# Kernel tuning notes

Hardware: AMD Instinct MI355X
Metric: run time of the kernel (lower is better)

Reference implementation:

```python
import jax, jax.numpy as jnp
import numpy as np

B, L, D = 4, 4096, 128
BLOCK, SPARSITY = 64, 0.9
NEG = -1e9


def _make_block_mask(key):
    nb = L // BLOCK
    bm = jax.random.uniform(key, (nb, nb)) > SPARSITY
    bm = bm | jnp.eye(nb, dtype=bool)  # keep diagonal blocks so no row is fully masked
    bm = jnp.tril(bm)
    return jnp.repeat(jnp.repeat(bm, BLOCK, axis=0), BLOCK, axis=1)  # [L, L]


def _xavier(key, shape):
    limit = float(np.sqrt(6.0 / (shape[0] + shape[1])))
    return jax.random.uniform(key, shape, jnp.float32, -limit, limit)


def setup_inputs() -> dict:
    key = jax.random.key(0)
    ks = jax.random.split(key, 10)
    t = lambda k: jax.random.normal(k, (B, L, D), jnp.float32)
    return {
        'q_real': t(ks[0]), 'q_imag': t(ks[1]),
        'k_real': t(ks[2]), 'k_imag': t(ks[3]),
        'v_real': t(ks[4]), 'v_imag': t(ks[5]),
        'W_qkv': _xavier(ks[6], (6 * D, 6 * D)),
        'b_qkv': jnp.zeros((6 * D,), jnp.float32),
        'W_out': _xavier(ks[7], (2 * D, 2 * D)),
        'b_out': jnp.zeros((2 * D,), jnp.float32),
        'block_mask': _make_block_mask(ks[8]),
    }


def reference(q_real, q_imag, k_real, k_imag, v_real, v_imag,
              W_qkv, b_qkv, W_out, b_out, block_mask):
    d = q_real.shape[-1]
    scale = d ** -0.5
    # fused qkv projection over the 6 concatenated channels
    x = jnp.concatenate([q_real, q_imag, k_real, k_imag, v_real, v_imag], axis=-1)  # [B,L,6D]
    qkv = (x @ W_qkv.T + b_qkv).reshape(x.shape[0], x.shape[1], 6, d)
    q_r, q_i, k_r, k_i, v_r, v_i = (qkv[:, :, j] for j in range(6))

    def attn(q, k, v):
        s = jnp.einsum('bqd,bkd->bqk', q, k) * scale          # [B,L,L]
        s = jnp.where(block_mask[None], s, NEG)               # block-sparse mask
        a = jax.nn.softmax(s, axis=-1)                        # dropout = identity (eval)
        return jnp.einsum('bqk,bkd->bqd', a, v)

    out = jnp.concatenate([attn(q_r, k_r, v_r), attn(q_i, k_i, v_i)], axis=-1)  # [B,L,2D]
    out = out @ W_out.T + b_out
    return out[..., :d], out[..., d:]
```

## Files before the change

### kernel.cpp

```cpp
#include <hip/hip_runtime.h>
#include <hip/hip_bf16.h>

typedef unsigned short u16;
typedef __attribute__((ext_vector_type(8))) short bf16x8;
typedef __attribute__((ext_vector_type(4))) float f32x4;

#define SEQ_L 4096
#define M_TOT 16384

__device__ __forceinline__ float bf2f(u16 x) {
    unsigned u = ((unsigned)x) << 16;
    return __builtin_bit_cast(float, u);
}
__device__ __forceinline__ u16 f2bf(float f) {
    unsigned u = __builtin_bit_cast(unsigned, f);
    u += 0x7FFFu + ((u >> 16) & 1u);
    return (u16)(u >> 16);
}
__device__ __forceinline__ void gload16(const u16* g, u16* l) {
    __builtin_amdgcn_global_load_lds(
        (const __attribute__((address_space(1))) unsigned int*)g,
        (__attribute__((address_space(3))) unsigned int*)l, 16, 0, 0);
}

__global__ __launch_bounds__(256) void prep_all(
    const float* __restrict__ in0, const float* __restrict__ in1, const float* __restrict__ in2,
    const float* __restrict__ in3, const float* __restrict__ in4, const float* __restrict__ in5,
    const float* __restrict__ Wqkv, const float* __restrict__ Wout, const void* __restrict__ mask,
    u16* __restrict__ x, u16* __restrict__ Wqkv_bf, u16* __restrict__ Wout_bf,
    unsigned long long* __restrict__ bmap) {
    int id = blockIdx.x * 256 + threadIdx.x;
    if (id < 1572864) {
        const float* ins[6] = {in0, in1, in2, in3, in4, in5};
        int which = id >> 18, j = id & 262143;
        int m = j >> 4, c8 = j & 15;
        const float* sp = ins[which] + (size_t)m * 128 + c8 * 8;
        float4 a = *(const float4*)sp;
        float4 b = *(const float4*)(sp + 4);
        u16 t[8] = {f2bf(a.x), f2bf(a.y), f2bf(a.z), f2bf(a.w),
                    f2bf(b.x), f2bf(b.y), f2bf(b.z), f2bf(b.w)};
        *(uint4*)(x + (size_t)m * 768 + which * 128 + c8 * 8) = *(uint4*)t;
    } else if (id < 1572864 + 73728 + 8192) {
        int i = id - 1572864;
        const float* src = (i < 73728) ? Wqkv : Wout;
        u16* dst = (i < 73728) ? Wqkv_bf : Wout_bf;
        if (i >= 73728) i -= 73728;
        const float* sp = src + (size_t)i * 8;
        float4 a = *(const float4*)sp;
        float4 b = *(const float4*)(sp + 4);
        u16 t[8] = {f2bf(a.x), f2bf(a.y), f2bf(a.z), f2bf(a.w),
                    f2bf(b.x), f2bf(b.y), f2bf(b.z), f2bf(b.w)};
        *(uint4*)(dst + (size_t)i * 8) = *(uint4*)t;
    } else if (id < 1572864 + 73728 + 8192 + 4096) {
        int i = id - 1572864 - 73728 - 8192;
        int bi = i >> 6, bj = i & 63;
        size_t e = (size_t)(bi * 64) * SEQ_L + (size_t)bj * 64;
        const unsigned char* p8 = (const unsigned char*)mask;
        unsigned w0 = *(const unsigned*)mask;
        bool v;
        if (w0 == 0x01010101u || w0 == 0xFFFFFFFFu)      v = p8[e] != 0;
        else if (w0 == 0x3F803F80u || w0 == 0x3C003C00u) v = ((const u16*)mask)[e] != 0;
        else                                             v = ((const unsigned*)mask)[e] != 0;
        unsigned long long bits = __ballot(v);
        if ((i & 63) == 0) bmap[bi] = bits;
    }
}

__global__ __launch_bounds__(256, 3) void qkv_gemm(
    const u16* __restrict__ X, const u16* __restrict__ W, const float* __restrict__ bias,
    u16* __restrict__ qk, u16* __restrict__ vt) {
    __shared__ __align__(16) u16 As[128 * 64];
    __shared__ __align__(16) u16 Bs[128 * 64];
    int m0 = blockIdx.x * 128, n0 = blockIdx.y * 128;
    int tid = threadIdx.x, lane = tid & 63, w = tid >> 6;
    int ln = lane & 15, quad = lane >> 4;
    int rw = (w >> 1) * 64, cw = (w & 1) * 64;
    int lr8 = lane >> 3, lc = lane & 7;
    f32x4 acc[4][4] = {};
    for (int kk = 0; kk < 768; kk += 64) {
        __syncthreads();
        #pragma unroll
        for (int j = 0; j < 4; j++) {
            int r0 = w * 32 + j * 8, r = r0 + lr8;
            gload16(X + (size_t)(m0 + r) * 768 + kk + ((lc ^ (r & 7)) * 8), As + r0 * 64 + lane * 8);
            gload16(W + (size_t)(n0 + r) * 768 + kk + ((lc ^ (r & 7)) * 8), Bs + r0 * 64 + lane * 8);
        }
        __syncthreads();
        #pragma unroll
        for (int s = 0; s < 2; s++) {
            bf16x8 af[4], bfr[4];
            #pragma unroll
            for (int i = 0; i < 4; i++) {
                int R = rw + i * 16 + ln;
                af[i] = *(const bf16x8*)(As + R * 64 + ((4 * s + quad) ^ (ln & 7)) * 8);
            }
            #pragma unroll
            for (int t = 0; t < 4; t++) {
                int R = cw + t * 16 + ln;
                bfr[t] = *(const bf16x8*)(Bs + R * 64 + ((4 * s + quad) ^ (ln & 7)) * 8);
            }
            #pragma unroll
            for (int i = 0; i < 4; i++)
                #pragma unroll
                for (int t = 0; t < 4; t++)
                    acc[i][t] = __builtin_amdgcn_mfma_f32_16x16x32_bf16(af[i], bfr[t], acc[i][t], 0, 0, 0);
        }
    }
    if (n0 < 512) {
        #pragma unroll
        for (int i = 0; i < 4; i++) {
            int row0 = m0 + rw + i * 16 + 4 * quad;
            #pragma unroll
            for (int t = 0; t < 4; t++) {
                int col = n0 + cw + t * 16 + ln;
                float bv = bias[col];
                #pragma unroll
                for (int r = 0; r < 4; r++)
                    qk[(size_t)(row0 + r) * 512 + col] = f2bf(acc[i][t][r] + bv);
            }
        }
    } else {
        #pragma unroll
        for (int i = 0; i < 4; i++) {
            int row0 = m0 + rw + i * 16 + 4 * quad;
            int b = row0 >> 12, seq = row0 & 4095;
            #pragma unroll
            for (int t = 0; t < 4; t++) {
                int col = n0 + cw + t * 16 + ln;
                float bv = bias[col];
                int d = col - 512;
                u16 pk[4] = {f2bf(acc[i][t][0] + bv), f2bf(acc[i][t][1] + bv),
                             f2bf(acc[i][t][2] + bv), f2bf(acc[i][t][3] + bv)};
                *(ushort4*)(vt + ((size_t)(b * 2 + (d >> 7)) * 128 + (d & 127)) * SEQ_L + seq)
                    = *(ushort4*)pk;
            }
        }
    }
}

__global__ __launch_bounds__(256, 2) void attn_sparse(
    const u16* __restrict__ qk, const u16* __restrict__ vt,
    const unsigned long long* __restrict__ bmap, u16* __restrict__ attn_bf) {
    __shared__ __align__(16) u16 Ks[2][64 * 128];
    __shared__ __align__(16) u16 Vs[2][128 * 64];

    int lane = threadIdx.x & 63, w = threadIdx.x >> 6;
    int ln = lane & 15, quad = lane >> 4;
    int u = blockIdx.x >> 3, v = blockIdx.x & 7;
    int qi = (u < 32) ? (63 - u) : (u - 32);
    int b = v >> 1, ch = v & 1;
    int rowbase = b * SEQ_L + qi * 64 + w * 16;
    const float scale = 0.08838834764831845f;

    bf16x8 qf[4];
    {
        const u16* qp = qk + (size_t)(rowbase + ln) * 512 + ch * 128;
        #pragma unroll
        for (int s = 0; s < 4; s++) qf[s] = *(const bf16x8*)(qp + 32 * s + 8 * quad);
    }

    float m_st = -1e30f, l_st = 0.f;
    f32x4 accO[8] = {};

    const u16* kbase0 = qk + (size_t)b * SEQ_L * 512 + 256 + ch * 128;
    const u16* vbase0 = vt + (size_t)(b * 2 + ch) * 128 * SEQ_L;
    unsigned long long bm = bmap[qi];

    int kb = __ffsll(bm) - 1; bm &= bm - 1;
    {
        const u16* kp = kbase0 + (size_t)(kb * 64) * 512;
        const u16* vp = vbase0 + kb * 64;
        #pragma unroll
        for (int j = 0; j < 4; j++) {
            int kr = w * 16 + j * 4 + (lane >> 4);
            gload16(kp + (size_t)kr * 512 + (((lane & 15) ^ (kr & 7)) * 8),
                    Ks[0] + (w * 16 + j * 4) * 128 + lane * 8);
        }
        #pragma unroll
        for (int j = 0; j < 4; j++) {
            int d = w * 32 + j * 8 + (lane >> 3);
            gload16(vp + (size_t)d * SEQ_L + (((lane & 7) ^ (d & 7)) * 8),
                    Vs[0] + (w * 32 + j * 8) * 64 + lane * 8);
        }
    }

    int srcA = ln + ((quad & 1) << 5);
    int srcB = srcA + 16;
    bool hi = (quad & 2) != 0;

    int bufc = 0;
    while (true) {
        int nkb = -1;
        if (bm) {
            nkb = __ffsll(bm) - 1; bm &= bm - 1;
            const u16* kp = kbase0 + (size_t)(nkb * 64) * 512;
            const u16* vp = vbase0 + nkb * 64;
            u16* Kd = Ks[bufc ^ 1];
            u16* Vd = Vs[bufc ^ 1];
            #pragma unroll
            for (int j = 0; j < 4; j++) {
                int kr = w * 16 + j * 4 + (lane >> 4);
                gload16(kp + (size_t)kr * 512 + (((lane & 15) ^ (kr & 7)) * 8),
                        Kd + (w * 16 + j * 4) * 128 + lane * 8);
            }
            #pragma unroll
            for (int j = 0; j < 4; j++) {
                int d = w * 32 + j * 8 + (lane >> 3);
                gload16(vp + (size_t)d * SEQ_L + (((lane & 7) ^ (d & 7)) * 8),
                        Vd + (w * 32 + j * 8) * 64 + lane * 8);
            }
        }
        if (nkb >= 0) __builtin_amdgcn_s_waitcnt(0x0F78);
        else          __builtin_amdgcn_s_waitcnt(0x0F70);
        __builtin_amdgcn_s_barrier();

        const u16* K = Ks[bufc];
        const u16* V = Vs[bufc];

        f32x4 accS[4] = {};
        #pragma unroll
        for (int s = 0; s < 4; s++)
            #pragma unroll
            for (int t = 0; t < 4; t++) {
                bf16x8 kf = *(const bf16x8*)(K + (t * 16 + ln) * 128 +
                                             (((4 * s + quad) ^ (ln & 7)) * 8));
                accS[t] = __builtin_amdgcn_mfma_f32_16x16x32_bf16(kf, qf[s], accS[t], 0, 0, 0);
            }

        float mx = fmaxf(fmaxf(fmaxf(accS[0][0], accS[0][1]), fmaxf(accS[0][2], accS[0][3])),
                         fmaxf(fmaxf(fmaxf(accS[1][0], accS[1][1]), fmaxf(accS[1][2], accS[1][3])),
                               fmaxf(fmaxf(fmaxf(accS[2][0], accS[2][1]), fmaxf(accS[2][2], accS[2][3])),
                                     fmaxf(fmaxf(accS[3][0], accS[3][1]), fmaxf(accS[3][2], accS[3][3])))));
        mx = fmaxf(mx, __shfl_xor(mx, 16, 64));
        mx = fmaxf(mx, __shfl_xor(mx, 32, 64));
        float nm = fmaxf(m_st, mx * scale);
        float alpha = __expf(m_st - nm);
        m_st = nm;

        float p[4][4];
        float rs = 0.f;
        #pragma unroll
        for (int t = 0; t < 4; t++)
            #pragma unroll
            for (int r = 0; r < 4; r++) {
                p[t][r] = __expf(accS[t][r] * scale - nm);
                rs += p[t][r];
            }
        rs += __shfl_xor(rs, 16, 64);
        rs += __shfl_xor(rs, 32, 64);
        l_st = l_st * alpha + rs;

        unsigned uA[4], uB[4];
        #pragma unroll
        for (int t = 0; t < 4; t++) {
            uA[t] = (unsigned)f2bf(p[t][0]) | ((unsigned)f2bf(p[t][1]) << 16);
            uB[t] = (unsigned)f2bf(p[t][2]) | ((unsigned)f2bf(p[t][3]) << 16);
        }

        float al[4];
        #pragma unroll
        for (int r = 0; r < 4; r++) al[r] = __shfl(alpha, 4 * quad + r, 64);
        #pragma unroll
        for (int nt = 0; nt < 8; nt++)
            #pragma unroll
            for (int r = 0; r < 4; r++) accO[nt][r] *= al[r];

        #pragma unroll
        for (int h = 0; h < 2; h++) {
            unsigned a0 = (unsigned)__shfl((int)uA[2 * h], srcA, 64);
            unsigned a1 = (unsigned)__shfl((int)uA[2 * h + 1], srcA, 64);
            unsigned b0 = (unsigned)__shfl((int)uB[2 * h], srcA, 64);
            unsigned b1 = (unsigned)__shfl((int)uB[2 * h + 1], srcA, 64);
            unsigned c0 = (unsigned)__shfl((int)uA[2 * h], srcB, 64);
            unsigned c1 = (unsigned)__shfl((int)uA[2 * h + 1], srcB, 64);
            unsigned d0 = (unsigned)__shfl((int)uB[2 * h], srcB, 64);
            unsigned d1 = (unsigned)__shfl((int)uB[2 * h + 1], srcB, 64);
            union { unsigned w4[4]; bf16x8 v; } pu;
            pu.w4[0] = hi ? a1 : a0;
            pu.w4[1] = hi ? b1 : b0;
            pu.w4[2] = hi ? c1 : c0;
            pu.w4[3] = hi ? d1 : d0;
            bf16x8 pf = pu.v;
            #pragma unroll
            for (int nt = 0; nt < 8; nt++) {
                bf16x8 vf = *(const bf16x8*)(V + (nt * 16 + ln) * 64 +
                                             (((4 * h + quad) ^ (ln & 7)) * 8));
                accO[nt] = __builtin_amdgcn_mfma_f32_16x16x32_bf16(pf, vf, accO[nt], 0, 0, 0);
            }
        }

        if (nkb < 0) break;
        __builtin_amdgcn_s_barrier();
        bufc ^= 1;
    }

    float linv = 1.0f / fmaxf(l_st, 1e-20f);
    float inv[4];
    #pragma unroll
    for (int r = 0; r < 4; r++) inv[r] = __shfl(linv, 4 * quad + r, 64);
    #pragma unroll
    for (int nt = 0; nt < 8; nt++)
        #pragma unroll
        for (int r = 0; r < 4; r++)
            attn_bf[(size_t)(rowbase + 4 * quad + r) * 256 + ch * 128 + nt * 16 + ln]
                = f2bf(accO[nt][r] * inv[r]);
}

__global__ __launch_bounds__(256) void out_gemm(
    const u16* __restrict__ A, const u16* __restrict__ W, const float* __restrict__ bias,
    float* __restrict__ out) {
    __shared__ __align__(16) u16 As[64 * 64];
    __shared__ __align__(16) u16 Bs[64 * 64];
    int m0 = blockIdx.x * 64, n0 = blockIdx.y * 64;
    int tid = threadIdx.x, lane = tid & 63, w = tid >> 6;
    int ln = lane & 15, quad = lane >> 4;
    int lr8 = lane >> 3, lc = lane & 7;
    int swz_st = lc ^ (lr8 & 7);
    f32x4 acc[4] = {};
    for (int kk = 0; kk < 256; kk += 64) {
        __syncthreads();
        #pragma unroll
        for (int j = 0; j < 2; j++) {
            int r0 = w * 16 + j * 8;
            int r = r0 + lr8;
            gload16(A + (size_t)(m0 + r) * 256 + kk + swz_st * 8, As + r0 * 64 + lane * 8);
            gload16(W + (size_t)(n0 + r) * 256 + kk + swz_st * 8, Bs + r0 * 64 + lane * 8);
        }
        __syncthreads();
        #pragma unroll
        for (int s = 0; s < 2; s++) {
            int R = w * 16 + ln;
            bf16x8 af = *(const bf16x8*)(As + R * 64 + ((4 * s + quad) ^ (ln & 7)) * 8);
            #pragma unroll
            for (int t = 0; t < 4; t++) {
                int Rb = t * 16 + ln;
                bf16x8 bfr = *(const bf16x8*)(Bs + Rb * 64 + ((4 * s + quad) ^ (ln & 7)) * 8);
                acc[t] = __builtin_amdgcn_mfma_f32_16x16x32_bf16(af, bfr, acc[t], 0, 0, 0);
            }
        }
    }
    const size_t half = (size_t)M_TOT * 128;
    #pragma unroll
    for (int t = 0; t < 4; t++) {
        int col = n0 + t * 16 + ln;
        float bv = bias[col];
        float* base = (col < 128) ? (out + col) : (out + half + (col - 128));
        #pragma unroll
        for (int r = 0; r < 4; r++) {
            int row = m0 + w * 16 + 4 * quad + r;
            base[(size_t)row * 128] = acc[t][r] + bv;
        }
    }
}

extern "C" void kernel_launch(void* const* d_in, const int* in_sizes, int n_in,
                              void* d_out, int out_size, void* d_ws, size_t ws_size,
                              hipStream_t stream) {
    char* ws = (char*)d_ws;
    u16* x_bf    = (u16*)ws;
    u16* qk_buf  = x_bf + (size_t)M_TOT * 768;
    u16* vt_buf  = qk_buf + (size_t)M_TOT * 512;
    u16* attn_bf = vt_buf + (size_t)1024 * SEQ_L;
    u16* Wqkv_bf = attn_bf + (size_t)M_TOT * 256;
    u16* Wout_bf = Wqkv_bf + 589824;
    unsigned long long* bmap = (unsigned long long*)(Wout_bf + 65536);

    hipLaunchKernelGGL(prep_all, dim3(6480), dim3(256), 0, stream,
                       (const float*)d_in[0], (const float*)d_in[1], (const float*)d_in[2],
                       (const float*)d_in[3], (const float*)d_in[4], (const float*)d_in[5],
                       (const float*)d_in[6], (const float*)d_in[8], d_in[10],
                       x_bf, Wqkv_bf, Wout_bf, bmap);
    hipLaunchKernelGGL(qkv_gemm, dim3(128, 6), dim3(256), 0, stream,
                       x_bf, Wqkv_bf, (const float*)d_in[7], qk_buf, vt_buf);
    hipLaunchKernelGGL(attn_sparse, dim3(512), dim3(256), 0, stream,
                       qk_buf, vt_buf, bmap, attn_bf);
    hipLaunchKernelGGL(out_gemm, dim3(256, 4), dim3(256), 0, stream,
                       attn_bf, Wout_bf, (const float*)d_in[9], (float*)d_out);
}
```

Measured before the change: 195.3 us.

## Fuse fp32-to-bf16 input conversion into QKV GEMM A-tile loads

The separate prep pass that converted the six fp32 input tensors into a concatenated bf16 X buffer is removed. The QKV GEMM now reads fp32 activations directly, converts them with packed bf16 conversion instructions and writes swizzled tiles into LDS. This avoids writing and re-reading a 24 MB intermediate. In exchange the A-tile load becomes synchronous register loads instead of async global-to-LDS copies, and each fp32 input is read six times (once per N block column) at twice the bytes.

```diff
diff --git a/kernel.cpp b/kernel.cpp
--- a/kernel.cpp
+++ b/kernel.cpp
@@ -17,6 +17,11 @@
     u += 0x7FFFu + ((u >> 16) & 1u);
     return (u16)(u >> 16);
 }
+__device__ __forceinline__ unsigned cvt_pk_bf16(float lo, float hi) {
+    unsigned r;
+    asm("v_cvt_pk_bf16_f32 %0, %1, %2" : "=v"(r) : "v"(lo), "v"(hi));
+    return r;
+}
 __device__ __forceinline__ void gload16(const u16* g, u16* l) {
     __builtin_amdgcn_global_load_lds(
         (const __attribute__((address_space(1))) unsigned int*)g,
@@ -24,24 +29,12 @@
 }
 
 __global__ __launch_bounds__(256) void prep_all(
-    const float* __restrict__ in0, const float* __restrict__ in1, const float* __restrict__ in2,
-    const float* __restrict__ in3, const float* __restrict__ in4, const float* __restrict__ in5,
     const float* __restrict__ Wqkv, const float* __restrict__ Wout, const void* __restrict__ mask,
-    u16* __restrict__ x, u16* __restrict__ Wqkv_bf, u16* __restrict__ Wout_bf,
+    u16* __restrict__ Wqkv_bf, u16* __restrict__ Wout_bf,
     unsigned long long* __restrict__ bmap) {
     int id = blockIdx.x * 256 + threadIdx.x;
-    if (id < 1572864) {
-        const float* ins[6] = {in0, in1, in2, in3, in4, in5};
-        int which = id >> 18, j = id & 262143;
-        int m = j >> 4, c8 = j & 15;
-        const float* sp = ins[which] + (size_t)m * 128 + c8 * 8;
-        float4 a = *(const float4*)sp;
-        float4 b = *(const float4*)(sp + 4);
-        u16 t[8] = {f2bf(a.x), f2bf(a.y), f2bf(a.z), f2bf(a.w),
-                    f2bf(b.x), f2bf(b.y), f2bf(b.z), f2bf(b.w)};
-        *(uint4*)(x + (size_t)m * 768 + which * 128 + c8 * 8) = *(uint4*)t;
-    } else if (id < 1572864 + 73728 + 8192) {
-        int i = id - 1572864;
+    if (id < 73728 + 8192) {
+        int i = id;
         const float* src = (i < 73728) ? Wqkv : Wout;
         u16* dst = (i < 73728) ? Wqkv_bf : Wout_bf;
         if (i >= 73728) i -= 73728;
@@ -51,8 +44,8 @@
         u16 t[8] = {f2bf(a.x), f2bf(a.y), f2bf(a.z), f2bf(a.w),
                     f2bf(b.x), f2bf(b.y), f2bf(b.z), f2bf(b.w)};
         *(uint4*)(dst + (size_t)i * 8) = *(uint4*)t;
-    } else if (id < 1572864 + 73728 + 8192 + 4096) {
-        int i = id - 1572864 - 73728 - 8192;
+    } else if (id < 73728 + 8192 + 4096) {
+        int i = id - 73728 - 8192;
         int bi = i >> 6, bj = i & 63;
         size_t e = (size_t)(bi * 64) * SEQ_L + (size_t)bj * 64;
         const unsigned char* p8 = (const unsigned char*)mask;
@@ -67,22 +60,45 @@
 }
 
 __global__ __launch_bounds__(256, 3) void qkv_gemm(
-    const u16* __restrict__ X, const u16* __restrict__ W, const float* __restrict__ bias,
+    const float* __restrict__ in0, const float* __restrict__ in1, const float* __restrict__ in2,
+    const float* __restrict__ in3, const float* __restrict__ in4, const float* __restrict__ in5,
+    const u16* __restrict__ W, const float* __restrict__ bias,
     u16* __restrict__ qk, u16* __restrict__ vt) {
     __shared__ __align__(16) u16 As[128 * 64];
     __shared__ __align__(16) u16 Bs[128 * 64];
+    const float* const XS[6] = {in0, in1, in2, in3, in4, in5};
     int m0 = blockIdx.x * 128, n0 = blockIdx.y * 128;
     int tid = threadIdx.x, lane = tid & 63, w = tid >> 6;
     int ln = lane & 15, quad = lane >> 4;
     int rw = (w >> 1) * 64, cw = (w & 1) * 64;
     int lr8 = lane >> 3, lc = lane & 7;
+    int arow = tid >> 1, ahalf = tid & 1;
     f32x4 acc[4][4] = {};
-    for (int kk = 0; kk < 768; kk += 64) {
+    #pragma unroll
+    for (int kk6 = 0; kk6 < 12; kk6++) {
+        const int kk = kk6 * 64;
+        const float* Xc = XS[kk6 >> 1];
+        const int koff = (kk6 & 1) * 64;
         __syncthreads();
+        {
+            const float* sp = Xc + (size_t)(m0 + arow) * 128 + koff + ahalf * 32;
+            float4 f[8];
+            #pragma unroll
+            for (int q = 0; q < 8; q++) f[q] = *(const float4*)(sp + q * 4);
+            #pragma unroll
+            for (int j = 0; j < 4; j++) {
+                unsigned pk[4] = {
+                    cvt_pk_bf16(f[2 * j].x, f[2 * j].y),
+                    cvt_pk_bf16(f[2 * j].z, f[2 * j].w),
+                    cvt_pk_bf16(f[2 * j + 1].x, f[2 * j + 1].y),
+                    cvt_pk_bf16(f[2 * j + 1].z, f[2 * j + 1].w)};
+                int c = ahalf * 4 + j;
+                *(uint4*)(As + arow * 64 + (c ^ (arow & 7)) * 8) = *(uint4*)pk;
+            }
+        }
         #pragma unroll
         for (int j = 0; j < 4; j++) {
             int r0 = w * 32 + j * 8, r = r0 + lr8;
-            gload16(X + (size_t)(m0 + r) * 768 + kk + ((lc ^ (r & 7)) * 8), As + r0 * 64 + lane * 8);
             gload16(W + (size_t)(n0 + r) * 768 + kk + ((lc ^ (r & 7)) * 8), Bs + r0 * 64 + lane * 8);
         }
         __syncthreads();
@@ -357,21 +373,20 @@
                               void* d_out, int out_size, void* d_ws, size_t ws_size,
                               hipStream_t stream) {
     char* ws = (char*)d_ws;
-    u16* x_bf    = (u16*)ws;
-    u16* qk_buf  = x_bf + (size_t)M_TOT * 768;
+    u16* qk_buf  = (u16*)ws;
     u16* vt_buf  = qk_buf + (size_t)M_TOT * 512;
     u16* attn_bf = vt_buf + (size_t)1024 * SEQ_L;
     u16* Wqkv_bf = attn_bf + (size_t)M_TOT * 256;
     u16* Wout_bf = Wqkv_bf + 589824;
     unsigned long long* bmap = (unsigned long long*)(Wout_bf + 65536);
 
-    hipLaunchKernelGGL(prep_all, dim3(6480), dim3(256), 0, stream,
+    hipLaunchKernelGGL(prep_all, dim3(336), dim3(256), 0, stream,
+                       (const float*)d_in[6], (const float*)d_in[8], d_in[10],
+                       Wqkv_bf, Wout_bf, bmap);
+    hipLaunchKernelGGL(qkv_gemm, dim3(128, 6), dim3(256), 0, stream,
                        (const float*)d_in[0], (const float*)d_in[1], (const float*)d_in[2],
                        (const float*)d_in[3], (const float*)d_in[4], (const float*)d_in[5],
-                       (const float*)d_in[6], (const float*)d_in[8], d_in[10],
-                       x_bf, Wqkv_bf, Wout_bf, bmap);
-    hipLaunchKernelGGL(qkv_gemm, dim3(128, 6), dim3(256), 0, stream,
-                       x_bf, Wqkv_bf, (const float*)d_in[7], qk_buf, vt_buf);
+                       Wqkv_bf, (const float*)d_in[7], qk_buf, vt_buf);
     hipLaunchKernelGGL(attn_sparse, dim3(512), dim3(256), 0, stream,
                        qk_buf, vt_buf, bmap, attn_bf);
     hipLaunchKernelGGL(out_gemm, dim3(256, 4), dim3(256), 0, stream,
```

Result: slower. 216.5 us (+10.9%).

## Split attention into 32-row query tiles with single-buffered K/V in smaller blocks

Applied to the files above, without the earlier changes.

The attention kernel now launches twice as many blocks, each with two waves covering 32 query rows instead of four waves covering 64. The double-buffered K/V prefetch pipeline is dropped in favour of a single buffer with a synchronous load, wait and compute per key block. The aim is more parallelism and occupancy: more blocks to balance the uneven causal-sparse work, and less LDS per block. In exchange, every K/V tile is loaded twice as often overall, and load latency is no longer overlapped with compute inside a block.

```diff
diff --git a/kernel.cpp b/kernel.cpp
--- a/kernel.cpp
+++ b/kernel.cpp
@@ -138,18 +138,18 @@
     }
 }
 
-__global__ __launch_bounds__(256, 2) void attn_sparse(
+__global__ __launch_bounds__(128, 4) void attn_sparse(
     const u16* __restrict__ qk, const u16* __restrict__ vt,
     const unsigned long long* __restrict__ bmap, u16* __restrict__ attn_bf) {
-    __shared__ __align__(16) u16 Ks[2][64 * 128];
-    __shared__ __align__(16) u16 Vs[2][128 * 64];
+    __shared__ __align__(16) u16 Ks[64 * 128];
+    __shared__ __align__(16) u16 Vs[128 * 64];
 
     int lane = threadIdx.x & 63, w = threadIdx.x >> 6;
     int ln = lane & 15, quad = lane >> 4;
     int u = blockIdx.x >> 3, v = blockIdx.x & 7;
-    int qi = (u < 32) ? (63 - u) : (u - 32);
+    int qi2 = (u < 64) ? (127 - u) : (u - 64);
     int b = v >> 1, ch = v & 1;
-    int rowbase = b * SEQ_L + qi * 64 + w * 16;
+    int rowbase = b * SEQ_L + qi2 * 32 + w * 16;
     const float scale = 0.08838834764831845f;
 
     bf16x8 qf[4];
@@ -164,65 +164,36 @@
 
     const u16* kbase0 = qk + (size_t)b * SEQ_L * 512 + 256 + ch * 128;
     const u16* vbase0 = vt + (size_t)(b * 2 + ch) * 128 * SEQ_L;
-    unsigned long long bm = bmap[qi];
-
-    int kb = __ffsll(bm) - 1; bm &= bm - 1;
-    {
-        const u16* kp = kbase0 + (size_t)(kb * 64) * 512;
-        const u16* vp = vbase0 + kb * 64;
-        #pragma unroll
-        for (int j = 0; j < 4; j++) {
-            int kr = w * 16 + j * 4 + (lane >> 4);
-            gload16(kp + (size_t)kr * 512 + (((lane & 15) ^ (kr & 7)) * 8),
-                    Ks[0] + (w * 16 + j * 4) * 128 + lane * 8);
-        }
-        #pragma unroll
-        for (int j = 0; j < 4; j++) {
-            int d = w * 32 + j * 8 + (lane >> 3);
-            gload16(vp + (size_t)d * SEQ_L + (((lane & 7) ^ (d & 7)) * 8),
-                    Vs[0] + (w * 32 + j * 8) * 64 + lane * 8);
-        }
-    }
+    unsigned long long bm = bmap[qi2 >> 1];
 
     int srcA = ln + ((quad & 1) << 5);
     int srcB = srcA + 16;
     bool hi = (quad & 2) != 0;
 
-    int bufc = 0;
-    while (true) {
-        int nkb = -1;
-        if (bm) {
-            nkb = __ffsll(bm) - 1; bm &= bm - 1;
-            const u16* kp = kbase0 + (size_t)(nkb * 64) * 512;
-            const u16* vp = vbase0 + nkb * 64;
-            u16* Kd = Ks[bufc ^ 1];
-            u16* Vd = Vs[bufc ^ 1];
-            #pragma unroll
-            for (int j = 0; j < 4; j++) {
-                int kr = w * 16 + j * 4 + (lane >> 4);
-                gload16(kp + (size_t)kr * 512 + (((lane & 15) ^ (kr & 7)) * 8),
-                        Kd + (w * 16 + j * 4) * 128 + lane * 8);
-            }
-            #pragma unroll
-            for (int j = 0; j < 4; j++) {
-                int d = w * 32 + j * 8 + (lane >> 3);
-                gload16(vp + (size_t)d * SEQ_L + (((lane & 7) ^ (d & 7)) * 8),
-                        Vd + (w * 32 + j * 8) * 64 + lane * 8);
-            }
-        }
-        if (nkb >= 0) __builtin_amdgcn_s_waitcnt(0x0F78);
-        else          __builtin_amdgcn_s_waitcnt(0x0F70);
-        __builtin_amdgcn_s_barrier();
-
-        const u16* K = Ks[bufc];
-        const u16* V = Vs[bufc];
+    while (bm) {
+        int kb = __ffsll(bm) - 1; bm &= bm - 1;
+        const u16* kp = kbase0 + (size_t)(kb * 64) * 512;
+        const u16* vp = vbase0 + kb * 64;
+        #pragma unroll
+        for (int j = 0; j < 8; j++) {
+            int kr = j * 8 + w * 4 + (lane >> 4);
+            gload16(kp + (size_t)kr * 512 + (((lane & 15) ^ (kr & 7)) * 8),
+                    Ks + (j * 8 + w * 4) * 128 + lane * 8);
+        }
+        #pragma unroll
+        for (int j = 0; j < 8; j++) {
+            int d = j * 16 + w * 8 + (lane >> 3);
+            gload16(vp + (size_t)d * SEQ_L + (((lane & 7) ^ (d & 7)) * 8),
+                    Vs + (j * 16 + w * 8) * 64 + lane * 8);
+        }
+        __syncthreads();
 
         f32x4 accS[4] = {};
         #pragma unroll
         for (int s = 0; s < 4; s++)
             #pragma unroll
             for (int t = 0; t < 4; t++) {
-                bf16x8 kf = *(const bf16x8*)(K + (t * 16 + ln) * 128 +
+                bf16x8 kf = *(const bf16x8*)(Ks + (t * 16 + ln) * 128 +
                                              (((4 * s + quad) ^ (ln & 7)) * 8));
                 accS[t] = __builtin_amdgcn_mfma_f32_16x16x32_bf16(kf, qf[s], accS[t], 0, 0, 0);
             }
@@ -283,15 +254,12 @@
             bf16x8 pf = pu.v;
             #pragma unroll
             for (int nt = 0; nt < 8; nt++) {
-                bf16x8 vf = *(const bf16x8*)(V + (nt * 16 + ln) * 64 +
+                bf16x8 vf = *(const bf16x8*)(Vs + (nt * 16 + ln) * 64 +
                                              (((4 * h + quad) ^ (ln & 7)) * 8));
                 accO[nt] = __builtin_amdgcn_mfma_f32_16x16x32_bf16(pf, vf, accO[nt], 0, 0, 0);
             }
         }
-
-        if (nkb < 0) break;
-        __builtin_amdgcn_s_barrier();
-        bufc ^= 1;
+        __syncthreads();
     }
 
     float linv = 1.0f / fmaxf(l_st, 1e-20f);
@@ -372,7 +340,7 @@
                        x_bf, Wqkv_bf, Wout_bf, bmap);
     hipLaunchKernelGGL(qkv_gemm, dim3(128, 6), dim3(256), 0, stream,
                        x_bf, Wqkv_bf, (const float*)d_in[7], qk_buf, vt_buf);
-    hipLaunchKernelGGL(attn_sparse, dim3(512), dim3(256), 0, stream,
+    hipLaunchKernelGGL(attn_sparse, dim3(1024), dim3(128), 0, stream,
                        qk_buf, vt_buf, bmap, attn_bf);
     hipLaunchKernelGGL(out_gemm, dim3(256, 4), dim3(256), 0, stream,
                        attn_bf, Wout_bf, (const float*)d_in[9], (float*)d_out);
```

Result: slower. 201.5 us (+3.2%).

## Load V fragments directly from global into registers, drop V LDS staging

Applied to the files above, without the earlier changes.

The attention kernel no longer stages V tiles in shared memory. Each wave now loads its V MFMA fragments straight from global memory into registers, issued after the QK MFMAs and during the softmax so their latency can overlap that work. Halving the LDS footprint allows the occupancy hint to rise from 2 to 3 blocks per CU. The cost is that every wave issues redundant global V loads with no LDS reuse across waves, uncoalesced 16-byte row accesses, and higher register pressure from 16 held fragments.

```diff
diff --git a/kernel.cpp b/kernel.cpp
--- a/kernel.cpp
+++ b/kernel.cpp
@@ -138,11 +138,10 @@
     }
 }
 
-__global__ __launch_bounds__(256, 2) void attn_sparse(
+__global__ __launch_bounds__(256, 3) void attn_sparse(
     const u16* __restrict__ qk, const u16* __restrict__ vt,
     const unsigned long long* __restrict__ bmap, u16* __restrict__ attn_bf) {
     __shared__ __align__(16) u16 Ks[2][64 * 128];
-    __shared__ __align__(16) u16 Vs[2][128 * 64];
 
     int lane = threadIdx.x & 63, w = threadIdx.x >> 6;
     int ln = lane & 15, quad = lane >> 4;
@@ -166,21 +165,14 @@
     const u16* vbase0 = vt + (size_t)(b * 2 + ch) * 128 * SEQ_L;
     unsigned long long bm = bmap[qi];
 
-    int kb = __ffsll(bm) - 1; bm &= bm - 1;
+    int cur = __ffsll(bm) - 1; bm &= bm - 1;
     {
-        const u16* kp = kbase0 + (size_t)(kb * 64) * 512;
-        const u16* vp = vbase0 + kb * 64;
+        const u16* kp = kbase0 + (size_t)(cur * 64) * 512;
         #pragma unroll
         for (int j = 0; j < 4; j++) {
             int kr = w * 16 + j * 4 + (lane >> 4);
             gload16(kp + (size_t)kr * 512 + (((lane & 15) ^ (kr & 7)) * 8),
                     Ks[0] + (w * 16 + j * 4) * 128 + lane * 8);
-        }
-        #pragma unroll
-        for (int j = 0; j < 4; j++) {
-            int d = w * 32 + j * 8 + (lane >> 3);
-            gload16(vp + (size_t)d * SEQ_L + (((lane & 7) ^ (d & 7)) * 8),
-                    Vs[0] + (w * 32 + j * 8) * 64 + lane * 8);
         }
     }
 
@@ -194,28 +186,19 @@
         if (bm) {
             nkb = __ffsll(bm) - 1; bm &= bm - 1;
             const u16* kp = kbase0 + (size_t)(nkb * 64) * 512;
-            const u16* vp = vbase0 + nkb * 64;
             u16* Kd = Ks[bufc ^ 1];
-            u16* Vd = Vs[bufc ^ 1];
             #pragma unroll
             for (int j = 0; j < 4; j++) {
                 int kr = w * 16 + j * 4 + (lane >> 4);
                 gload16(kp + (size_t)kr * 512 + (((lane & 15) ^ (kr & 7)) * 8),
                         Kd + (w * 16 + j * 4) * 128 + lane * 8);
             }
-            #pragma unroll
-            for (int j = 0; j < 4; j++) {
-                int d = w * 32 + j * 8 + (lane >> 3);
-                gload16(vp + (size_t)d * SEQ_L + (((lane & 7) ^ (d & 7)) * 8),
-                        Vd + (w * 32 + j * 8) * 64 + lane * 8);
-            }
-        }
-        if (nkb >= 0) __builtin_amdgcn_s_waitcnt(0x0F78);
+        }
+        if (nkb >= 0) __builtin_amdgcn_s_waitcnt(0x0F74);
         else          __builtin_amdgcn_s_waitcnt(0x0F70);
         __builtin_amdgcn_s_barrier();
 
         const u16* K = Ks[bufc];
-        const u16* V = Vs[bufc];
 
         f32x4 accS[4] = {};
         #pragma unroll
@@ -226,6 +209,12 @@
                                              (((4 * s + quad) ^ (ln & 7)) * 8));
                 accS[t] = __builtin_amdgcn_mfma_f32_16x16x32_bf16(kf, qf[s], accS[t], 0, 0, 0);
             }
+
+        const u16* vkb = vbase0 + cur * 64;
+        bf16x8 vf0[8];
+        #pragma unroll
+        for (int nt = 0; nt < 8; nt++)
+            vf0[nt] = *(const bf16x8*)(vkb + (size_t)(nt * 16 + ln) * SEQ_L + quad * 8);
 
         float mx = fmaxf(fmaxf(fmaxf(accS[0][0], accS[0][1]), fmaxf(accS[0][2], accS[0][3])),
                          fmaxf(fmaxf(fmaxf(accS[1][0], accS[1][1]), fmaxf(accS[1][2], accS[1][3])),
@@ -250,6 +239,11 @@
         rs += __shfl_xor(rs, 32, 64);
         l_st = l_st * alpha + rs;
 
+        bf16x8 vf1[8];
+        #pragma unroll
+        for (int nt = 0; nt < 8; nt++)
+            vf1[nt] = *(const bf16x8*)(vkb + (size_t)(nt * 16 + ln) * SEQ_L + 32 + quad * 8);
+
         unsigned uA[4], uB[4];
         #pragma unroll
         for (int t = 0; t < 4; t++) {
@@ -265,16 +259,15 @@
             #pragma unroll
             for (int r = 0; r < 4; r++) accO[nt][r] *= al[r];
 
-        #pragma unroll
-        for (int h = 0; h < 2; h++) {
-            unsigned a0 = (unsigned)__shfl((int)uA[2 * h], srcA, 64);
-            unsigned a1 = (unsigned)__shfl((int)uA[2 * h + 1], srcA, 64);
-            unsigned b0 = (unsigned)__shfl((int)uB[2 * h], srcA, 64);
-            unsigned b1 = (unsigned)__shfl((int)uB[2 * h + 1], srcA, 64);
-            unsigned c0 = (unsigned)__shfl((int)uA[2 * h], srcB, 64);
-            unsigned c1 = (unsigned)__shfl((int)uA[2 * h + 1], srcB, 64);
-            unsigned d0 = (unsigned)__shfl((int)uB[2 * h], srcB, 64);
-            unsigned d1 = (unsigned)__shfl((int)uB[2 * h + 1], srcB, 64);
+        {
+            unsigned a0 = (unsigned)__shfl((int)uA[0], srcA, 64);
+            unsigned a1 = (unsigned)__shfl((int)uA[1], srcA, 64);
+            unsigned b0 = (unsigned)__shfl((int)uB[0], srcA, 64);
+            unsigned b1 = (unsigned)__shfl((int)uB[1], srcA, 64);
+            unsigned c0 = (unsigned)__shfl((int)uA[0], srcB, 64);
+            unsigned c1 = (unsigned)__shfl((int)uA[1], srcB, 64);
+            unsigned d0 = (unsigned)__shfl((int)uB[0], srcB, 64);
+            unsigned d1 = (unsigned)__shfl((int)uB[1], srcB, 64);
             union { unsigned w4[4]; bf16x8 v; } pu;
             pu.w4[0] = hi ? a1 : a0;
             pu.w4[1] = hi ? b1 : b0;
@@ -282,16 +275,33 @@
             pu.w4[3] = hi ? d1 : d0;
             bf16x8 pf = pu.v;
             #pragma unroll
-            for (int nt = 0; nt < 8; nt++) {
-                bf16x8 vf = *(const bf16x8*)(V + (nt * 16 + ln) * 64 +
-                                             (((4 * h + quad) ^ (ln & 7)) * 8));
-                accO[nt] = __builtin_amdgcn_mfma_f32_16x16x32_bf16(pf, vf, accO[nt], 0, 0, 0);
-            }
+            for (int nt = 0; nt < 8; nt++)
+                accO[nt] = __builtin_amdgcn_mfma_f32_16x16x32_bf16(pf, vf0[nt], accO[nt], 0, 0, 0);
+        }
+        {
+            unsigned a0 = (unsigned)__shfl((int)uA[2], srcA, 64);
+            unsigned a1 = (unsigned)__shfl((int)uA[3], srcA, 64);
+            unsigned b0 = (unsigned)__shfl((int)uB[2], srcA, 64);
+            unsigned b1 = (unsigned)__shfl((int)uB[3], srcA, 64);
+            unsigned c0 = (unsigned)__shfl((int)uA[2], srcB, 64);
+            unsigned c1 = (unsigned)__shfl((int)uA[3], srcB, 64);
+            unsigned d0 = (unsigned)__shfl((int)uB[2], srcB, 64);
+            unsigned d1 = (unsigned)__shfl((int)uB[3], srcB, 64);
+            union { unsigned w4[4]; bf16x8 v; } pu;
+            pu.w4[0] = hi ? a1 : a0;
+            pu.w4[1] = hi ? b1 : b0;
+            pu.w4[2] = hi ? c1 : c0;
+            pu.w4[3] = hi ? d1 : d0;
+            bf16x8 pf = pu.v;
+            #pragma unroll
+            for (int nt = 0; nt < 8; nt++)
+                accO[nt] = __builtin_amdgcn_mfma_f32_16x16x32_bf16(pf, vf1[nt], accO[nt], 0, 0, 0);
         }
 
         if (nkb < 0) break;
         __builtin_amdgcn_s_barrier();
         bufc ^= 1;
+        cur = nkb;
     }
 
     float linv = 1.0f / fmaxf(l_st, 1e-20f);
```

Result: slower. 219.1 us (+12.2%).
